# Kernel optimization log

Hardware: AMD Instinct MI355X
Metric: run time of the kernel (lower is better)

Reference implementation:

```python
import jax, jax.numpy as jnp
import numpy as np

N, E, H, D, L, R = 50000, 800000, 128, 512, 3, 3
BN_EPS = 1e-5


def setup_inputs() -> dict:
    key = jax.random.key(0)
    ks = jax.random.split(key, 10)
    x = jax.random.normal(ks[0], (N, H), jnp.float32)
    edge_src = jax.random.randint(ks[1], (R, E), 0, N, jnp.int32)
    edge_dst = jax.random.randint(ks[2], (R, E), 0, N, jnp.int32)
    conv_W = jax.random.normal(ks[3], (L, R, H, H), jnp.float32) * 0.05
    conv_b = jnp.zeros((L, R, H), jnp.float32)
    fc_W = jax.random.normal(ks[4], (L - 1, H, H), jnp.float32) * 0.05
    fc_b = jnp.zeros((L - 1, H), jnp.float32)
    fc_W_last = jax.random.normal(ks[5], (H, D), jnp.float32) * 0.05
    fc_b_last = jnp.zeros((D,), jnp.float32)
    bn_gamma = jnp.ones((L - 1, H), jnp.float32)
    bn_beta = jnp.zeros((L - 1, H), jnp.float32)
    bn_mean = jax.random.normal(ks[6], (L - 1, H), jnp.float32) * 0.1
    bn_var = jax.random.uniform(ks[7], (L - 1, H), jnp.float32, 0.5, 1.5)
    return {"x": x, "edge_src": edge_src, "edge_dst": edge_dst,
            "conv_W": conv_W, "conv_b": conv_b, "fc_W": fc_W, "fc_b": fc_b,
            "fc_W_last": fc_W_last, "fc_b_last": fc_b_last,
            "bn_gamma": bn_gamma, "bn_beta": bn_beta,
            "bn_mean": bn_mean, "bn_var": bn_var}


def _deg_norm(idx, n, dtype):
    # symmetric GCN norm: 1/sqrt(clamp(deg,1))  (DGL norm='both')
    deg = jax.ops.segment_sum(jnp.ones(idx.shape, dtype), idx, num_segments=n)
    return jax.lax.rsqrt(jnp.maximum(deg, 1.0))


def reference(x, edge_src, edge_dst, conv_W, conv_b, fc_W, fc_b,
              fc_W_last, fc_b_last, bn_gamma, bn_beta, bn_mean, bn_var):
    n = x.shape[0]
    # per-relation degree norms (graph fixed across layers)
    norm_out = [_deg_norm(edge_src[r], n, x.dtype) for r in range(R)]  # src side
    norm_in = [_deg_norm(edge_dst[r], n, x.dtype) for r in range(R)]   # dst side

    for l in range(L):
        # HeteroGraphConv: sum of 3 relation-wise GraphConvs
        h = jnp.zeros((n, conv_W.shape[-1]), x.dtype)
        for r in range(R):
            m = (x * norm_out[r][:, None]) @ conv_W[l, r]          # [N,H] transform first
            agg = jax.ops.segment_sum(m[edge_src[r]], edge_dst[r], num_segments=n)
            h = h + agg * norm_in[r][:, None] + conv_b[l, r]
        if l != L - 1:
            x = h @ fc_W[l] + fc_b[l]
            x = jax.nn.relu(x)
            # BatchNorm1d in eval mode (running stats); dropout = identity in eval
            x = bn_gamma[l] * (x - bn_mean[l]) * jax.lax.rsqrt(bn_var[l] + BN_EPS) + bn_beta[l]
        else:
            x = h @ fc_W_last + fc_b_last
    return x
```

## Files before the change

### kernel.cpp

```cpp
#include <hip/hip_runtime.h>

#define NN 50000
#define EE 800000
#define RR 3
#define HH 128
#define CAP 64
#define NB 128
#define BW 391
#define SEGCAP 8192

typedef __attribute__((ext_vector_type(8))) short short8;
typedef __attribute__((ext_vector_type(4))) float f32x4;
typedef unsigned short u16;
typedef unsigned int u32;

__device__ __forceinline__ float b2f(u16 u){
  unsigned v = ((unsigned)u) << 16;
  return __builtin_bit_cast(float, v);
}
__device__ __forceinline__ u16 f2bu(float f){
  unsigned u = __builtin_bit_cast(unsigned, f);
  u += 0x7fffu + ((u >> 16) & 1u);
  return (u16)(u >> 16);
}

__global__ __launch_bounds__(256) void init_k(int* __restrict__ cnts, int* __restrict__ bktcur,
                                              u32* __restrict__ xb32, u32* __restrict__ act32){
  int i = blockIdx.x * 256 + threadIdx.x;
  if (i < 2 * RR * NN) cnts[i] = 0;
  if (i < RR * NB) bktcur[i] = 0;
  if (i < 64) xb32[(size_t)NN * 64 + i] = 0;
  else if (i < 128) act32[(size_t)NN * 64 + (i - 64)] = 0;
}

__global__ __launch_bounds__(256) void bucket_p1(const int* __restrict__ src, const int* __restrict__ dst,
                                                 int* __restrict__ bktcur, u32* __restrict__ bktbuf,
                                                 int* __restrict__ cnt_out){
  __shared__ int h[RR * NB];
  __shared__ int basebk[RR * NB];
  int tid = threadIdx.x;
  for (int k = tid; k < RR * NB; k += 256) h[k] = 0;
  __syncthreads();

  int e0 = (blockIdx.x * 256 + tid) * 4;
  int kk[4] = {-1, -1, -1, -1}, rk[4] = {0,0,0,0}, sv[4] = {0,0,0,0};
  if (e0 < RR * EE){
    int4 s4 = ((const int4*)src)[e0 >> 2];
    int4 d4 = ((const int4*)dst)[e0 >> 2];
    int ss[4] = {s4.x, s4.y, s4.z, s4.w};
    int dd[4] = {d4.x, d4.y, d4.z, d4.w};
#pragma unroll
    for (int j = 0; j < 4; ++j){
      int e = e0 + j;
      int r = e / EE;
      atomicAdd(&cnt_out[r * NN + ss[j]], 1);
      int b = dd[j] / BW;
      kk[j] = r * NB + b;
      sv[j] = ss[j] | ((dd[j] - b * BW) << 16);
      rk[j] = atomicAdd(&h[kk[j]], 1);
    }
  }
  __syncthreads();
  for (int k = tid; k < RR * NB; k += 256){
    int c = h[k];
    basebk[k] = c ? atomicAdd(&bktcur[k], c) : 0;
  }
  __syncthreads();
#pragma unroll
  for (int j = 0; j < 4; ++j){
    if (kk[j] >= 0){
      int pos = basebk[kk[j]] + rk[j];
      if (pos < SEGCAP) bktbuf[(size_t)kk[j] * SEGCAP + pos] = (u32)sv[j];
    }
  }
}

__global__ __launch_bounds__(256) void slots_p2(const int* __restrict__ bktcur, const u32* __restrict__ bktbuf,
                                                u16* __restrict__ slots, int* __restrict__ cnt_in){
  __shared__ int cur[BW];
  int k = blockIdx.x, tid = threadIdx.x;
  int r = k / NB, b = k % NB, d0 = b * BW;
  for (int i = tid; i < BW; i += 256) cur[i] = 0;
  __syncthreads();
  int n = bktcur[k]; if (n > SEGCAP) n = SEGCAP;
  const u32* buf = bktbuf + (size_t)k * SEGCAP;
  for (int t = tid; t < n; t += 256){
    u32 pl = buf[t];
    int dl = (int)(pl >> 16), s = (int)(pl & 0xffffu);
    int p = atomicAdd(&cur[dl], 1);
    if (p < CAP) slots[((size_t)r * NN + d0 + dl) * CAP + p] = (u16)s;
  }
  __syncthreads();
  for (int i = tid; i < BW; i += 256){
    int d = d0 + i;
    if (d < NN) cnt_in[r * NN + d] = cur[i];
  }
}

__global__ __launch_bounds__(256) void norms2_k(const int* __restrict__ cin, const int* __restrict__ cout_,
                                                float* __restrict__ nin, float* __restrict__ nout,
                                                u16* __restrict__ slots){
  int i = blockIdx.x * 256 + threadIdx.x;
  if (i >= RR * NN) return;
  int a = cin[i];
  int c = a; if (c > CAP) c = CAP;
  int n8 = (c + 7) & ~7;
  u16* sl = slots + (size_t)i * CAP;
  for (int p = c; p < n8; ++p) sl[p] = (u16)NN;
  if (a < 1) a = 1;
  int b = cout_[i]; if (b < 1) b = 1;
  nin[i] = rsqrtf((float)a);
  nout[i] = rsqrtf((float)b);
  if (i == 0) nout[RR * NN] = 1.0f;
}

__global__ __launch_bounds__(256) void cvt_bf16(const float* __restrict__ in, u16* __restrict__ out, int n4){
  int i = blockIdx.x * 256 + threadIdx.x;
  if (i >= n4) return;
  float4 v = ((const float4*)in)[i];
  ushort4 o; o.x = f2bu(v.x); o.y = f2bu(v.y); o.z = f2bu(v.z); o.w = f2bu(v.w);
  ((ushort4*)out)[i] = o;
}

__global__ __launch_bounds__(256) void pack_bf(const float* __restrict__ B, u16* __restrict__ Bp,
                                               int K, int nc, int total){
  int i = blockIdx.x * 256 + threadIdx.x;
  if (i >= total) return;
  int per = K * nc;
  int b = i / per, rem = i % per;
  int k = rem / nc, n = rem % nc;
  Bp[b * per + ((k >> 3) * nc + n) * 8 + (k & 7)] = f2bu(B[i]);
}

__global__ __launch_bounds__(256) void gather_agg(
    const u16* __restrict__ xin, const u16* __restrict__ slots,
    const int* __restrict__ cin, const float* __restrict__ nin,
    const float* __restrict__ nout, u16* __restrict__ agg)
{
  int tid = threadIdx.x;
  int lane = tid & 63;
  int ql = lane & 15;
  int qb = lane & 48;
  int r = blockIdx.y;
  int row = blockIdx.x * 16 + (tid >> 4);
  int rNN = r * NN;
  const u16* sl = slots + ((size_t)rNN + row) * CAP;
  int cnt = cin[rNN + row]; if (cnt > CAP) cnt = CAP;
  int n8 = (cnt + 7) & ~7;
  float a[8];
#pragma unroll
  for (int k = 0; k < 8; ++k) a[k] = 0.f;

  for (int base = 0; base < n8; base += 16){
    u32 w = (u32)sl[base + ql];
#pragma unroll
    for (int gstep = 0; gstep < 16; gstep += 8){
      if (base + gstep < n8){
        int uu[8]; float cf[8]; short8 vv[8];
#pragma unroll
        for (int j = 0; j < 8; ++j)
          uu[j] = __shfl((int)w, qb + gstep + j);
#pragma unroll
        for (int j = 0; j < 8; ++j)
          vv[j] = *(const short8*)(xin + (size_t)uu[j] * HH + ql * 8);
#pragma unroll
        for (int j = 0; j < 8; ++j)
          cf[j] = nout[rNN + uu[j]];
#pragma unroll
        for (int j = 0; j < 8; ++j){
          float c = cf[j];
#pragma unroll
          for (int k = 0; k < 8; ++k)
            a[k] += c * b2f((u16)vv[j][k]);
        }
      }
    }
  }
  float sc = nin[rNN + row];
  short8 o;
#pragma unroll
  for (int k = 0; k < 8; ++k) o[k] = (short)f2bu(sc * a[k]);
  *(short8*)(agg + ((size_t)rNN + row) * HH + ql * 8) = o;
}

template<int MODE>
__global__ __launch_bounds__(256) void dense_layer(
    const u16* __restrict__ agg,
    const u16* __restrict__ Wc, const float* __restrict__ bc,
    const u16* __restrict__ Wf, const float* __restrict__ bfc,
    const float* __restrict__ g, const float* __restrict__ be,
    const float* __restrict__ mu, const float* __restrict__ va,
    u16* __restrict__ out_bf, float* __restrict__ out_f)
{
  __shared__ u16 tile[64][136];
  int tid = threadIdx.x, wave = tid >> 6, lane = tid & 63;
  int q = lane >> 4, l15 = lane & 15;
  int nb = blockIdx.x * 64;
  f32x4 zf = {0.f, 0.f, 0.f, 0.f};
  f32x4 acc[8];
#pragma unroll
  for (int ct = 0; ct < 8; ++ct) acc[ct] = zf;

  for (int r = 0; r < RR; ++r){
#pragma unroll
    for (int p = 0; p < 4; ++p){
      int chunk = p * 256 + tid;
      int rw = chunk >> 4, cc = chunk & 15;
      int node = nb + rw;
      if (node >= NN) node = NN - 1;
      short8 v = *(const short8*)(agg + ((size_t)r * NN + node) * HH + cc * 8);
      *(short8*)&tile[rw][cc * 8] = v;
    }
    __syncthreads();
    const short8* bp = (const short8*)(Wc + (size_t)r * HH * HH);
#pragma unroll
    for (int kb = 0; kb < 4; ++kb){
      short8 a = *(const short8*)&tile[wave * 16 + l15][kb * 32 + q * 8];
#pragma unroll
      for (int ct = 0; ct < 8; ++ct){
        short8 b = bp[(kb * 4 + q) * HH + ct * 16 + l15];
        acc[ct] = __builtin_amdgcn_mfma_f32_16x16x32_bf16(a, b, acc[ct], 0, 0, 0);
      }
    }
    __syncthreads();
  }

#pragma unroll
  for (int ct = 0; ct < 8; ++ct){
    int col = ct * 16 + l15;
    float badd = bc[col] + bc[HH + col] + bc[2 * HH + col];
#pragma unroll
    for (int i = 0; i < 4; ++i)
      tile[wave * 16 + q * 4 + i][col] = f2bu(acc[ct][i] + badd);
  }
  __syncthreads();

  if (MODE == 0){
    f32x4 a2[8];
#pragma unroll
    for (int ct = 0; ct < 8; ++ct) a2[ct] = zf;
    const short8* bp = (const short8*)Wf;
#pragma unroll
    for (int kb = 0; kb < 4; ++kb){
      short8 a = *(const short8*)&tile[wave * 16 + l15][kb * 32 + q * 8];
#pragma unroll
      for (int ct = 0; ct < 8; ++ct){
        short8 b = bp[(kb * 4 + q) * HH + ct * 16 + l15];
        a2[ct] = __builtin_amdgcn_mfma_f32_16x16x32_bf16(a, b, a2[ct], 0, 0, 0);
      }
    }
#pragma unroll
    for (int ct = 0; ct < 8; ++ct){
      int col = ct * 16 + l15;
      float bb = bfc[col];
      float s0 = g[col] * rsqrtf(va[col] + 1e-5f);
      float m0 = mu[col], b0 = be[col];
#pragma unroll
      for (int i = 0; i < 4; ++i){
        int node = nb + wave * 16 + q * 4 + i;
        if (node < NN){
          float v = a2[ct][i] + bb;
          v = fmaxf(v, 0.f);
          v = (v - m0) * s0 + b0;
          out_bf[(size_t)node * HH + col] = f2bu(v);
        }
      }
    }
  } else {
    f32x4 a2[4][8];
#pragma unroll
    for (int rt = 0; rt < 4; ++rt)
#pragma unroll
      for (int ct = 0; ct < 8; ++ct) a2[rt][ct] = zf;
    const short8* bp = (const short8*)Wf;
#pragma unroll
    for (int kb = 0; kb < 4; ++kb){
      int cbase = (kb * 4 + q) * 512 + wave * 128;
#pragma unroll
      for (int rt = 0; rt < 4; ++rt){
        short8 a = *(const short8*)&tile[rt * 16 + l15][kb * 32 + q * 8];
#pragma unroll
        for (int ct = 0; ct < 8; ++ct){
          short8 b = bp[cbase + ct * 16 + l15];
          a2[rt][ct] = __builtin_amdgcn_mfma_f32_16x16x32_bf16(a, b, a2[rt][ct], 0, 0, 0);
        }
      }
    }
#pragma unroll
    for (int rt = 0; rt < 4; ++rt)
#pragma unroll
    for (int ct = 0; ct < 8; ++ct){
      int col = wave * 128 + ct * 16 + l15;
      float bb = bfc[col];
#pragma unroll
      for (int i = 0; i < 4; ++i){
        int node = nb + rt * 16 + q * 4 + i;
        if (node < NN) out_f[(size_t)node * 512 + col] = a2[rt][ct][i] + bb;
      }
    }
  }
}

extern "C" void kernel_launch(void* const* d_in, const int* in_sizes, int n_in,
                              void* d_out, int out_size, void* d_ws, size_t ws_size,
                              hipStream_t stream){
  const float* x_in  = (const float*)d_in[0];
  const int* esrc    = (const int*)d_in[1];
  const int* edst    = (const int*)d_in[2];
  const float* convW = (const float*)d_in[3];
  const float* convB = (const float*)d_in[4];
  const float* fcW   = (const float*)d_in[5];
  const float* fcB   = (const float*)d_in[6];
  const float* fcWl  = (const float*)d_in[7];
  const float* fcBl  = (const float*)d_in[8];
  const float* bng   = (const float*)d_in[9];
  const float* bnb   = (const float*)d_in[10];
  const float* bnm   = (const float*)d_in[11];
  const float* bnv   = (const float*)d_in[12];

  char* w = (char*)d_ws;
  size_t off = 0;
  auto alloc = [&](size_t bytes) -> char* {
    char* p = w + off;
    off += (bytes + 255) & ~(size_t)255;
    return p;
  };
  int* cnts    = (int*)alloc((size_t)2 * RR * NN * 4);
  int* bktcur  = (int*)alloc((size_t)RR * NB * 4);
  u32* bktbuf  = (u32*)alloc((size_t)RR * NB * SEGCAP * 4);
  float* nin   = (float*)alloc((size_t)RR * NN * 4);
  float* nout  = (float*)alloc((size_t)(RR * NN + 1) * 4);
  u16* slots   = (u16*)alloc((size_t)RR * NN * CAP * 2);
  u16* xb      = (u16*)alloc((size_t)(NN + 1) * HH * 2);
  u16* act     = (u16*)alloc((size_t)(NN + 1) * HH * 2);
  u16* agg     = (u16*)alloc((size_t)RR * NN * HH * 2);
  u16* convWp  = (u16*)alloc((size_t)3 * 384 * 128 * 2);
  u16* fcWp    = (u16*)alloc((size_t)2 * 128 * 128 * 2);
  u16* fcWlp   = (u16*)alloc((size_t)128 * 512 * 2);

  int* cnt_in  = cnts;
  int* cnt_out = cnts + (size_t)RR * NN;

  const int TPB = 256;
  init_k<<<(2 * RR * NN + TPB - 1) / TPB, TPB, 0, stream>>>(cnts, bktcur, (u32*)xb, (u32*)act);
  bucket_p1<<<(RR * EE / 4 + TPB - 1) / TPB, TPB, 0, stream>>>(esrc, edst, bktcur, bktbuf, cnt_out);
  slots_p2<<<RR * NB, TPB, 0, stream>>>(bktcur, bktbuf, slots, cnt_in);
  norms2_k<<<(RR * NN + TPB - 1) / TPB, TPB, 0, stream>>>(cnt_in, cnt_out, nin, nout, slots);
  cvt_bf16<<<(NN * HH / 4 + TPB - 1) / TPB, TPB, 0, stream>>>(x_in, xb, NN * HH / 4);
  pack_bf<<<(3 * 384 * 128 + TPB - 1) / TPB, TPB, 0, stream>>>(convW, convWp, 384, 128, 3 * 384 * 128);
  pack_bf<<<(2 * 128 * 128 + TPB - 1) / TPB, TPB, 0, stream>>>(fcW, fcWp, 128, 128, 2 * 128 * 128);
  pack_bf<<<(128 * 512 + TPB - 1) / TPB, TPB, 0, stream>>>(fcWl, fcWlp, 128, 512, 128 * 512);

  int gx = (NN + 63) / 64;
  dim3 ggrid(NN / 16, RR);

  gather_agg<<<ggrid, TPB, 0, stream>>>(xb, slots, cnt_in, nin, nout, agg);
  dense_layer<0><<<gx, TPB, 0, stream>>>(agg,
      convWp + (size_t)0 * 384 * 128, convB + 0 * 384,
      fcWp + (size_t)0 * 128 * 128, fcB + 0 * 128,
      bng + 0 * 128, bnb + 0 * 128, bnm + 0 * 128, bnv + 0 * 128, act, nullptr);
  gather_agg<<<ggrid, TPB, 0, stream>>>(act, slots, cnt_in, nin, nout, agg);
  dense_layer<0><<<gx, TPB, 0, stream>>>(agg,
      convWp + (size_t)1 * 384 * 128, convB + 1 * 384,
      fcWp + (size_t)1 * 128 * 128, fcB + 1 * 128,
      bng + 1 * 128, bnb + 1 * 128, bnm + 1 * 128, bnv + 1 * 128, act, nullptr);
  gather_agg<<<ggrid, TPB, 0, stream>>>(act, slots, cnt_in, nin, nout, agg);
  dense_layer<1><<<gx, TPB, 0, stream>>>(agg,
      convWp + (size_t)2 * 384 * 128, convB + 2 * 384,
      fcWlp, fcBl,
      nullptr, nullptr, nullptr, nullptr, nullptr, (float*)d_out);
}
```

Measured before the change: 655.7 us.

## Replace global-atomic edge bucketing with per-block sub-buckets and overflow lists

Edge bucketing now writes each block's entries into fixed per-(bucket,block) sub-buckets of 32 slots, with a small global overflow list for the rest. This removes the global bucket-cursor atomics and the per-edge global atomics used for out-degree counting. Out-degree is now computed by a new histogram pass over source buckets, and buffers are aliased so agg/xb/act reuse the bucket memory. The gather loop also prefetches the next slot word one iteration ahead. In exchange the second-pass kernels scan a larger, sparse set of sub-buckets serially per thread and filter the overflow list in every block.

```diff
diff --git a/kernel.cpp b/kernel.cpp
--- a/kernel.cpp
+++ b/kernel.cpp
@@ -7,12 +7,15 @@
 #define CAP 64
 #define NB 128
 #define BW 391
-#define SEGCAP 8192
+#define NBLK 1172
+#define SCB 32
+#define OVCAP 4096
 
 typedef __attribute__((ext_vector_type(8))) short short8;
 typedef __attribute__((ext_vector_type(4))) float f32x4;
 typedef unsigned short u16;
 typedef unsigned int u32;
+typedef unsigned long long u64;
 
 __device__ __forceinline__ float b2f(u16 u){
   unsigned v = ((unsigned)u) << 16;
@@ -24,71 +27,91 @@
   return (u16)(u >> 16);
 }
 
-__global__ __launch_bounds__(256) void init_k(int* __restrict__ cnts, int* __restrict__ bktcur,
-                                              u32* __restrict__ xb32, u32* __restrict__ act32){
-  int i = blockIdx.x * 256 + threadIdx.x;
-  if (i < 2 * RR * NN) cnts[i] = 0;
-  if (i < RR * NB) bktcur[i] = 0;
+__global__ __launch_bounds__(128) void init_k(u32* __restrict__ xb32, u32* __restrict__ act32){
+  int i = threadIdx.x;
   if (i < 64) xb32[(size_t)NN * 64 + i] = 0;
-  else if (i < 128) act32[(size_t)NN * 64 + (i - 64)] = 0;
+  else act32[(size_t)NN * 64 + (i - 64)] = 0;
 }
 
 __global__ __launch_bounds__(256) void bucket_p1(const int* __restrict__ src, const int* __restrict__ dst,
-                                                 int* __restrict__ bktcur, u32* __restrict__ bktbuf,
-                                                 int* __restrict__ cnt_out){
-  __shared__ int h[RR * NB];
-  __shared__ int basebk[RR * NB];
-  int tid = threadIdx.x;
-  for (int k = tid; k < RR * NB; k += 256) h[k] = 0;
-  __syncthreads();
-
-  int e0 = (blockIdx.x * 256 + tid) * 4;
-  int kk[4] = {-1, -1, -1, -1}, rk[4] = {0,0,0,0}, sv[4] = {0,0,0,0};
+                                                 u32* __restrict__ bktd, u16* __restrict__ bkts,
+                                                 int* __restrict__ cnt_d, int* __restrict__ cnt_s,
+                                                 u64* __restrict__ ovd, u32* __restrict__ ovs,
+                                                 int* __restrict__ ovcur){
+  __shared__ int hd[RR * NB];
+  __shared__ int hs[RR * NB];
+  int tid = threadIdx.x, blk = blockIdx.x;
+  for (int k = tid; k < RR * NB; k += 256){ hd[k] = 0; hs[k] = 0; }
+  __syncthreads();
+
+  int e0 = (blk * 256 + tid) * 8;
   if (e0 < RR * EE){
-    int4 s4 = ((const int4*)src)[e0 >> 2];
-    int4 d4 = ((const int4*)dst)[e0 >> 2];
-    int ss[4] = {s4.x, s4.y, s4.z, s4.w};
-    int dd[4] = {d4.x, d4.y, d4.z, d4.w};
-#pragma unroll
-    for (int j = 0; j < 4; ++j){
-      int e = e0 + j;
-      int r = e / EE;
-      atomicAdd(&cnt_out[r * NN + ss[j]], 1);
-      int b = dd[j] / BW;
-      kk[j] = r * NB + b;
-      sv[j] = ss[j] | ((dd[j] - b * BW) << 16);
-      rk[j] = atomicAdd(&h[kk[j]], 1);
+    int r = e0 / EE;
+#pragma unroll
+    for (int h = 0; h < 2; ++h){
+      int4 s4 = ((const int4*)src)[(e0 >> 2) + h];
+      int4 d4 = ((const int4*)dst)[(e0 >> 2) + h];
+      int ss[4] = {s4.x, s4.y, s4.z, s4.w};
+      int dd[4] = {d4.x, d4.y, d4.z, d4.w};
+#pragma unroll
+      for (int j = 0; j < 4; ++j){
+        int bd = dd[j] / BW;
+        int kd = r * NB + bd;
+        u32 sv = (u32)ss[j] | ((u32)(dd[j] - bd * BW) << 16);
+        int rk = atomicAdd(&hd[kd], 1);
+        if (rk < SCB)
+          bktd[((size_t)kd * NBLK + blk) * SCB + rk] = sv;
+        else {
+          int p = atomicAdd(&ovcur[0], 1);
+          if (p < OVCAP) ovd[p] = ((u64)kd << 32) | (u64)sv;
+        }
+        int bs = ss[j] / BW;
+        int ks = r * NB + bs;
+        u16 sloc = (u16)(ss[j] - bs * BW);
+        int rs = atomicAdd(&hs[ks], 1);
+        if (rs < SCB)
+          bkts[((size_t)ks * NBLK + blk) * SCB + rs] = sloc;
+        else {
+          int p = atomicAdd(&ovcur[1], 1);
+          if (p < OVCAP) ovs[p] = ((u32)ks << 16) | (u32)sloc;
+        }
+      }
     }
   }
   __syncthreads();
   for (int k = tid; k < RR * NB; k += 256){
-    int c = h[k];
-    basebk[k] = c ? atomicAdd(&bktcur[k], c) : 0;
-  }
-  __syncthreads();
-#pragma unroll
-  for (int j = 0; j < 4; ++j){
-    if (kk[j] >= 0){
-      int pos = basebk[kk[j]] + rk[j];
-      if (pos < SEGCAP) bktbuf[(size_t)kk[j] * SEGCAP + pos] = (u32)sv[j];
-    }
-  }
-}
-
-__global__ __launch_bounds__(256) void slots_p2(const int* __restrict__ bktcur, const u32* __restrict__ bktbuf,
+    cnt_d[blk * (RR * NB) + k] = hd[k];
+    cnt_s[blk * (RR * NB) + k] = hs[k];
+  }
+}
+
+__global__ __launch_bounds__(256) void slots_p2(const int* __restrict__ cnt_d, const u32* __restrict__ bktd,
+                                                const u64* __restrict__ ovd, const int* __restrict__ ovcur,
                                                 u16* __restrict__ slots, int* __restrict__ cnt_in){
   __shared__ int cur[BW];
   int k = blockIdx.x, tid = threadIdx.x;
   int r = k / NB, b = k % NB, d0 = b * BW;
   for (int i = tid; i < BW; i += 256) cur[i] = 0;
   __syncthreads();
-  int n = bktcur[k]; if (n > SEGCAP) n = SEGCAP;
-  const u32* buf = bktbuf + (size_t)k * SEGCAP;
-  for (int t = tid; t < n; t += 256){
-    u32 pl = buf[t];
-    int dl = (int)(pl >> 16), s = (int)(pl & 0xffffu);
-    int p = atomicAdd(&cur[dl], 1);
-    if (p < CAP) slots[((size_t)r * NN + d0 + dl) * CAP + p] = (u16)s;
+  for (int blk = tid; blk < NBLK; blk += 256){
+    int c = cnt_d[blk * (RR * NB) + k]; if (c > SCB) c = SCB;
+    const u32* buf = bktd + ((size_t)k * NBLK + blk) * SCB;
+    for (int t = 0; t < c; ++t){
+      u32 pl = buf[t];
+      int dl = (int)(pl >> 16), s = (int)(pl & 0xffffu);
+      int p = atomicAdd(&cur[dl], 1);
+      if (p < CAP) slots[((size_t)r * NN + d0 + dl) * CAP + p] = (u16)s;
+    }
+  }
+  int nov = ovcur[0]; if (nov > OVCAP) nov = OVCAP;
+  for (int t = tid; t < nov; t += 256){
+    u64 e = ovd[t];
+    if ((int)(e >> 32) == k){
+      u32 pl = (u32)e;
+      int dl = (int)(pl >> 16), s = (int)(pl & 0xffffu);
+      int p = atomicAdd(&cur[dl], 1);
+      if (p < CAP) slots[((size_t)r * NN + d0 + dl) * CAP + p] = (u16)s;
+    }
   }
   __syncthreads();
   for (int i = tid; i < BW; i += 256){
@@ -97,7 +120,37 @@
   }
 }
 
-__global__ __launch_bounds__(256) void norms2_k(const int* __restrict__ cin, const int* __restrict__ cout_,
+__global__ __launch_bounds__(256) void hist_p2(const int* __restrict__ cnt_s, const u16* __restrict__ bkts,
+                                               const u32* __restrict__ ovs, const int* __restrict__ ovcur,
+                                               float* __restrict__ nout){
+  __shared__ int cur[BW];
+  int k = blockIdx.x, tid = threadIdx.x;
+  int r = k / NB, b = k % NB, d0 = b * BW;
+  for (int i = tid; i < BW; i += 256) cur[i] = 0;
+  __syncthreads();
+  for (int blk = tid; blk < NBLK; blk += 256){
+    int c = cnt_s[blk * (RR * NB) + k]; if (c > SCB) c = SCB;
+    const u16* buf = bkts + ((size_t)k * NBLK + blk) * SCB;
+    for (int t = 0; t < c; ++t)
+      atomicAdd(&cur[buf[t]], 1);
+  }
+  int nov = ovcur[1]; if (nov > OVCAP) nov = OVCAP;
+  for (int t = tid; t < nov; t += 256){
+    u32 e = ovs[t];
+    if ((int)(e >> 16) == k)
+      atomicAdd(&cur[e & 0xffffu], 1);
+  }
+  __syncthreads();
+  for (int i = tid; i < BW; i += 256){
+    int s = d0 + i;
+    if (s < NN){
+      int c = cur[i]; if (c < 1) c = 1;
+      nout[r * NN + s] = rsqrtf((float)c);
+    }
+  }
+}
+
+__global__ __launch_bounds__(256) void norms2_k(const int* __restrict__ cin,
                                                 float* __restrict__ nin, float* __restrict__ nout,
                                                 u16* __restrict__ slots){
   int i = blockIdx.x * 256 + threadIdx.x;
@@ -108,9 +161,7 @@
   u16* sl = slots + (size_t)i * CAP;
   for (int p = c; p < n8; ++p) sl[p] = (u16)NN;
   if (a < 1) a = 1;
-  int b = cout_[i]; if (b < 1) b = 1;
   nin[i] = rsqrtf((float)a);
-  nout[i] = rsqrtf((float)b);
   if (i == 0) nout[RR * NN] = 1.0f;
 }
 
@@ -151,8 +202,10 @@
 #pragma unroll
   for (int k = 0; k < 8; ++k) a[k] = 0.f;
 
+  u32 w = (u32)sl[ql];
   for (int base = 0; base < n8; base += 16){
-    u32 w = (u32)sl[base + ql];
+    u32 wn = 0u;
+    if (base + 16 < n8) wn = (u32)sl[base + 16 + ql];
 #pragma unroll
     for (int gstep = 0; gstep < 16; gstep += 8){
       if (base + gstep < n8){
@@ -175,6 +228,7 @@
         }
       }
     }
+    w = wn;
   }
   float sc = nin[rNN + row];
   short8 o;
@@ -325,27 +379,37 @@
     off += (bytes + 255) & ~(size_t)255;
     return p;
   };
-  int* cnts    = (int*)alloc((size_t)2 * RR * NN * 4);
-  int* bktcur  = (int*)alloc((size_t)RR * NB * 4);
-  u32* bktbuf  = (u32*)alloc((size_t)RR * NB * SEGCAP * 4);
+  size_t BKTD_B = (size_t)RR * NB * NBLK * SCB * 4;
+  size_t BKTS_B = (size_t)RR * NB * NBLK * SCB * 2;
+  size_t AGG_B  = (size_t)RR * NN * HH * 2;
+  size_t XB_B   = (size_t)(NN + 1) * HH * 2;
+  char* regionA = alloc(BKTD_B + BKTS_B);
+  u32* bktd = (u32*)regionA;
+  u16* bkts = (u16*)(regionA + BKTD_B);
+  u16* agg  = (u16*)regionA;
+  u16* xb   = (u16*)(regionA + ((AGG_B + 255) & ~(size_t)255));
+  u16* act  = (u16*)(regionA + ((AGG_B + XB_B + 511) & ~(size_t)255));
+
+  int* cnt_d   = (int*)alloc((size_t)NBLK * RR * NB * 4);
+  int* cnt_s   = (int*)alloc((size_t)NBLK * RR * NB * 4);
+  int* cnt_in  = (int*)alloc((size_t)RR * NN * 4);
   float* nin   = (float*)alloc((size_t)RR * NN * 4);
   float* nout  = (float*)alloc((size_t)(RR * NN + 1) * 4);
   u16* slots   = (u16*)alloc((size_t)RR * NN * CAP * 2);
-  u16* xb      = (u16*)alloc((size_t)(NN + 1) * HH * 2);
-  u16* act     = (u16*)alloc((size_t)(NN + 1) * HH * 2);
-  u16* agg     = (u16*)alloc((size_t)RR * NN * HH * 2);
+  u64* ovd     = (u64*)alloc((size_t)OVCAP * 8);
+  u32* ovs     = (u32*)alloc((size_t)OVCAP * 4);
+  int* ovcur   = (int*)alloc(256);
   u16* convWp  = (u16*)alloc((size_t)3 * 384 * 128 * 2);
   u16* fcWp    = (u16*)alloc((size_t)2 * 128 * 128 * 2);
   u16* fcWlp   = (u16*)alloc((size_t)128 * 512 * 2);
 
-  int* cnt_in  = cnts;
-  int* cnt_out = cnts + (size_t)RR * NN;
-
   const int TPB = 256;
-  init_k<<<(2 * RR * NN + TPB - 1) / TPB, TPB, 0, stream>>>(cnts, bktcur, (u32*)xb, (u32*)act);
-  bucket_p1<<<(RR * EE / 4 + TPB - 1) / TPB, TPB, 0, stream>>>(esrc, edst, bktcur, bktbuf, cnt_out);
-  slots_p2<<<RR * NB, TPB, 0, stream>>>(bktcur, bktbuf, slots, cnt_in);
-  norms2_k<<<(RR * NN + TPB - 1) / TPB, TPB, 0, stream>>>(cnt_in, cnt_out, nin, nout, slots);
+  hipMemsetAsync(ovcur, 0, 8, stream);
+  bucket_p1<<<NBLK, TPB, 0, stream>>>(esrc, edst, bktd, bkts, cnt_d, cnt_s, ovd, ovs, ovcur);
+  slots_p2<<<RR * NB, TPB, 0, stream>>>(cnt_d, bktd, ovd, ovcur, slots, cnt_in);
+  hist_p2<<<RR * NB, TPB, 0, stream>>>(cnt_s, bkts, ovs, ovcur, nout);
+  norms2_k<<<(RR * NN + TPB - 1) / TPB, TPB, 0, stream>>>(cnt_in, nin, nout, slots);
+  init_k<<<1, 128, 0, stream>>>((u32*)xb, (u32*)act);
   cvt_bf16<<<(NN * HH / 4 + TPB - 1) / TPB, TPB, 0, stream>>>(x_in, xb, NN * HH / 4);
   pack_bf<<<(3 * 384 * 128 + TPB - 1) / TPB, TPB, 0, stream>>>(convW, convWp, 384, 128, 3 * 384 * 128);
   pack_bf<<<(2 * 128 * 128 + TPB - 1) / TPB, TPB, 0, stream>>>(fcW, fcWp, 128, 128, 2 * 128 * 128);
```

New measurement: 601.0 us. 1.09x faster.
